# Optimization experiments

Hardware: AMD Instinct MI355X
Metric: run time of the kernel (lower is better)

Reference implementation:

```python
import jax, jax.numpy as jnp
import numpy as np

B, N, C, H, F = 4, 256, 256, 8, 64  # batch, nodes, in_channels, heads, n_hidden


def setup_inputs() -> dict:
    key = jax.random.key(0)
    k1, k2, k3, k4, k5 = jax.random.split(key, 5)
    x = jax.random.normal(k1, (B, N, C), jnp.float32)
    W_l = jax.random.normal(k2, (C, H * F), jnp.float32) / np.sqrt(C)
    W_r = jax.random.normal(k3, (C, H * F), jnp.float32) / np.sqrt(C)
    attn_w = jax.random.normal(k4, (F,), jnp.float32) / np.sqrt(F)
    adj = jax.random.randint(k5, (N, N, H), 0, 2, jnp.int32)
    # guarantee at least one unmasked head per (i, j) pair so the
    # softmax-over-heads (dim=-1 in the source) never sees all -inf
    adj = adj.at[:, :, 0].set(1)
    return {"x": x, "W_l": W_l, "W_r": W_r, "attn_w": attn_w, "adj": adj}


def reference(x, W_l, W_r, attn_w, adj):
    b, n, _ = x.shape
    g_l = (x @ W_l).reshape(b, n, H, F)
    g_r = (x @ W_r).reshape(b, n, H, F)
    # torch: g_l.repeat(1,n,1,1) + g_r.repeat_interleave(n,dim=1), then
    # view(b,n,n,h,f)  =>  g_sum[b,i,j,h,f] = g_r[b,i] + g_l[b,j]
    g_sum = g_r[:, :, None] + g_l[:, None, :]          # [b,i,j,h,f]
    e = jnp.einsum('bijhf,f->bijh', jax.nn.leaky_relu(g_sum, 0.2), attn_w)
    e = jnp.where(adj == 0, -jnp.inf, e)               # adj broadcasts over batch
    a = jax.nn.softmax(e, axis=-1)                     # softmax over heads, per source (dim=-1)
    out = jnp.einsum('bijh,bjhf->bihf', a, g_r)        # aggregate over neighbors j
    return out.reshape(b, n, H * F)                    # is_concat=True
```

## Files before the change

### kernel.cpp

```cpp
#include <hip/hip_runtime.h>
#include <hip/hip_bf16.h>

typedef _Float16 h2 __attribute__((ext_vector_type(2)));

constexpr int kB = 4, kN = 256, kC = 256, kH = 8, kF = 64, kHF = 512;
constexpr int kIPB = 4;
constexpr int kJS = 2;

union H2U { h2 h; unsigned int u; };

__global__ __launch_bounds__(256) void gat_gemm_kernel(
    const float* __restrict__ x,
    const float* __restrict__ Wl,
    const float* __restrict__ Wr,
    unsigned int* __restrict__ gl,
    unsigned int* __restrict__ gr,
    float* __restrict__ out)
{
    __shared__ float xs[4][kC];
    const int rowBase = blockIdx.x * 4;
    const float* Wm = (blockIdx.y == 0) ? Wl : Wr;
    unsigned int* gout = (blockIdx.y == 0) ? gl : gr;

    const int tid = threadIdx.x;

    if (blockIdx.y == 0) {
        float4 z = make_float4(0.f, 0.f, 0.f, 0.f);
        float4* o = (float4*)out + blockIdx.x * 512 + tid * 2;
        o[0] = z; o[1] = z;
    }

    {
        const int r = tid >> 6;
        const int kc = (tid & 63) * 4;
        *(float4*)&xs[r][kc] = *(const float4*)(x + (rowBase + r) * kC + kc);
    }
    __syncthreads();

    const int c0 = tid * 2;
    float acc[4][2];
#pragma unroll
    for (int r = 0; r < 4; ++r) { acc[r][0] = 0.f; acc[r][1] = 0.f; }

    float2 wv[4], wn[4];
#pragma unroll
    for (int kk = 0; kk < 4; ++kk)
        wv[kk] = *(const float2*)(Wm + kk * kHF + c0);

    for (int k = 0; k < kC; k += 4) {
        if (k + 4 < kC) {
#pragma unroll
            for (int kk = 0; kk < 4; ++kk)
                wn[kk] = *(const float2*)(Wm + (k + 4 + kk) * kHF + c0);
        }
#pragma unroll
        for (int r = 0; r < 4; ++r) {
            float4 xv = *(const float4*)&xs[r][k];
            acc[r][0] = fmaf(xv.x, wv[0].x, acc[r][0]);
            acc[r][1] = fmaf(xv.x, wv[0].y, acc[r][1]);
            acc[r][0] = fmaf(xv.y, wv[1].x, acc[r][0]);
            acc[r][1] = fmaf(xv.y, wv[1].y, acc[r][1]);
            acc[r][0] = fmaf(xv.z, wv[2].x, acc[r][0]);
            acc[r][1] = fmaf(xv.z, wv[2].y, acc[r][1]);
            acc[r][0] = fmaf(xv.w, wv[3].x, acc[r][0]);
            acc[r][1] = fmaf(xv.w, wv[3].y, acc[r][1]);
        }
#pragma unroll
        for (int kk = 0; kk < 4; ++kk) wv[kk] = wn[kk];
    }

#pragma unroll
    for (int r = 0; r < 4; ++r) {
        H2U p; p.h = (h2){(_Float16)acc[r][0], (_Float16)acc[r][1]};
        gout[((rowBase + r) * kHF + c0) >> 1] = p.u;
    }
}

__global__ __launch_bounds__(1024, 8) void gat_attn_kernel(
    const unsigned int* __restrict__ gl,
    const unsigned int* __restrict__ gr,
    const float* __restrict__ attn_w,
    const int* __restrict__ adj,
    float* __restrict__ out)
{
    __shared__ float red[8 * kIPB * kHF];
    __shared__ unsigned int msk[kN / kJS];

    const int bi0 = blockIdx.x * kIPB;
    const int i0 = bi0 & 255;
    const int j0 = blockIdx.y * (kN / kJS);
    const int tid = threadIdx.x;
    const int wv = tid >> 6;
    const int lane = tid & 63;
    const int h = lane >> 3;
    const int fg = lane & 7;

    if (tid < 512) {
        const int jj = tid & 127;
        const int ii = tid >> 7;
        const int* ap = adj + (i0 + ii) * (kN * kH) + (j0 + jj) * kH;
        uint4 a0 = *(const uint4*)ap;
        uint4 a1 = *(const uint4*)(ap + 4);
        unsigned int m = 0;
        m |= (a0.x != 0) << 0; m |= (a0.y != 0) << 1;
        m |= (a0.z != 0) << 2; m |= (a0.w != 0) << 3;
        m |= (a1.x != 0) << 4; m |= (a1.y != 0) << 5;
        m |= (a1.z != 0) << 6; m |= (a1.w != 0) << 7;
        ((unsigned char*)msk)[jj * 4 + ii] = (unsigned char)m;
    }

    h2 gri[kIPB][4];
#pragma unroll
    for (int ii = 0; ii < kIPB; ++ii) {
        uint4 pk = *(const uint4*)(gr + ((bi0 + ii) * 256 + h * 32 + fg * 4));
        H2U a0, a1, a2, a3;
        a0.u = pk.x; a1.u = pk.y; a2.u = pk.z; a3.u = pk.w;
        gri[ii][0] = a0.h; gri[ii][1] = a1.h; gri[ii][2] = a2.h; gri[ii][3] = a3.h;
    }
    h2 w2[4];
    {
        float4 wa = *(const float4*)(attn_w + fg * 8);
        float4 wb = *(const float4*)(attn_w + fg * 8 + 4);
        w2[0] = (h2){(_Float16)wa.x, (_Float16)wa.y};
        w2[1] = (h2){(_Float16)wa.z, (_Float16)wa.w};
        w2[2] = (h2){(_Float16)wb.x, (_Float16)wb.y};
        w2[3] = (h2){(_Float16)wb.z, (_Float16)wb.w};
    }

    h2 acc[kIPB][4];
#pragma unroll
    for (int ii = 0; ii < kIPB; ++ii)
#pragma unroll
        for (int q = 0; q < 4; ++q) acc[ii][q] = (h2){(_Float16)0.f, (_Float16)0.f};

    const h2 c02 = (h2){(_Float16)0.2f, (_Float16)0.2f};

    __syncthreads();

    unsigned int goff = (unsigned int)((bi0 >> 8) * (kN * 256)
                                       + (j0 + wv) * 256 + h * 32 + fg * 4);

    for (int it = 0; it < kN / kJS / 16; ++it) {
        const int jl = wv + it * 16;
        uint4 ga = *(const uint4*)(gl + goff);
        uint4 gb = *(const uint4*)(gr + goff);
        goff += 16 * 256;
        const unsigned int m = msk[jl];

        h2 gl2[4], gr2[4];
        { H2U t; t.u = ga.x; gl2[0] = t.h; t.u = ga.y; gl2[1] = t.h;
                 t.u = ga.z; gl2[2] = t.h; t.u = ga.w; gl2[3] = t.h;
                 t.u = gb.x; gr2[0] = t.h; t.u = gb.y; gr2[1] = t.h;
                 t.u = gb.z; gr2[2] = t.h; t.u = gb.w; gr2[3] = t.h; }

#pragma unroll
        for (int ii = 0; ii < kIPB; ++ii) {
            float e = 0.f;
#pragma unroll
            for (int q = 0; q < 4; ++q) {
                h2 s = gri[ii][q] + gl2[q];
                h2 u = __builtin_elementwise_max(s, c02 * s);
                e = __builtin_amdgcn_fdot2(u, w2[q], e, false);
            }
            e += __shfl_xor(e, 1);
            e += __shfl_xor(e, 2);
            e += __shfl_xor(e, 4);

            const unsigned int bit = (m >> (ii * 8 + h)) & 1u;
            e = bit ? e : -1e30f;

            float ex = __expf(e);
            float den = ex;
            den += __shfl_xor(den, 8);
            den += __shfl_xor(den, 16);
            den += __shfl_xor(den, 32);
            float a = ex * __builtin_amdgcn_rcpf(den);

            const h2 a2 = (h2){(_Float16)a, (_Float16)a};
#pragma unroll
            for (int q = 0; q < 4; ++q)
                acc[ii][q] = __builtin_elementwise_fma(a2, gr2[q], acc[ii][q]);
        }
    }

    if (wv >= 8) {
#pragma unroll
        for (int ii = 0; ii < kIPB; ++ii) {
            float* rp = &red[((wv - 8) * kIPB + ii) * kHF + lane * 8];
#pragma unroll
            for (int q = 0; q < 4; ++q) {
                float2 f = make_float2((float)acc[ii][q].x, (float)acc[ii][q].y);
                *(float2*)&rp[q * 2] = f;
            }
        }
    }
    __syncthreads();
    if (wv < 8) {
#pragma unroll
        for (int ii = 0; ii < kIPB; ++ii) {
            float* rp = &red[(wv * kIPB + ii) * kHF + lane * 8];
#pragma unroll
            for (int q = 0; q < 4; ++q) {
                float2 f = *(float2*)&rp[q * 2];
                f.x += (float)acc[ii][q].x;
                f.y += (float)acc[ii][q].y;
                *(float2*)&rp[q * 2] = f;
            }
        }
    }
    __syncthreads();

#pragma unroll
    for (int t = tid; t < kIPB * kHF; t += 1024) {
        const int ii = t >> 9;
        const int c  = t & 511;
        float s = 0.f;
#pragma unroll
        for (int w8 = 0; w8 < 8; ++w8)
            s += red[(w8 * kIPB + ii) * kHF + c];
        atomicAdd(&out[(bi0 + ii) * kHF + c], s);
    }
}

extern "C" void kernel_launch(void* const* d_in, const int* in_sizes, int n_in,
                              void* d_out, int out_size, void* d_ws, size_t ws_size,
                              hipStream_t stream) {
    const float* x  = (const float*)d_in[0];
    const float* Wl = (const float*)d_in[1];
    const float* Wr = (const float*)d_in[2];
    const float* aw = (const float*)d_in[3];
    const int* adj  = (const int*)d_in[4];

    unsigned int* gl = (unsigned int*)d_ws;
    unsigned int* gr = gl + (size_t)kB * kN * kHF / 2;

    dim3 g1(kB * kN / 4, 2);
    gat_gemm_kernel<<<g1, 256, 0, stream>>>(x, Wl, Wr, gl, gr, (float*)d_out);

    dim3 g2(kB * kN / kIPB, kJS);
    gat_attn_kernel<<<g2, 1024, 0, stream>>>(
        gl, gr, aw, adj, (float*)d_out);
}
```

Measured before the change: 112.7 us.

## Drop j-split and atomics in attention kernel; read x directly in GEMM

```diff
diff --git a/kernel.cpp b/kernel.cpp
--- a/kernel.cpp
+++ b/kernel.cpp
@@ -4,8 +4,7 @@
 typedef _Float16 h2 __attribute__((ext_vector_type(2)));
 
 constexpr int kB = 4, kN = 256, kC = 256, kH = 8, kF = 64, kHF = 512;
-constexpr int kIPB = 4;
-constexpr int kJS = 2;
+constexpr int kIPB = 2;
 
 union H2U { h2 h; unsigned int u; };
 
@@ -14,59 +13,41 @@
     const float* __restrict__ Wl,
     const float* __restrict__ Wr,
     unsigned int* __restrict__ gl,
-    unsigned int* __restrict__ gr,
-    float* __restrict__ out)
+    unsigned int* __restrict__ gr)
 {
-    __shared__ float xs[4][kC];
     const int rowBase = blockIdx.x * 4;
     const float* Wm = (blockIdx.y == 0) ? Wl : Wr;
     unsigned int* gout = (blockIdx.y == 0) ? gl : gr;
 
     const int tid = threadIdx.x;
-
-    if (blockIdx.y == 0) {
-        float4 z = make_float4(0.f, 0.f, 0.f, 0.f);
-        float4* o = (float4*)out + blockIdx.x * 512 + tid * 2;
-        o[0] = z; o[1] = z;
-    }
-
-    {
-        const int r = tid >> 6;
-        const int kc = (tid & 63) * 4;
-        *(float4*)&xs[r][kc] = *(const float4*)(x + (rowBase + r) * kC + kc);
-    }
-    __syncthreads();
-
     const int c0 = tid * 2;
+    const float* xr = x + rowBase * kC;
+
     float acc[4][2];
 #pragma unroll
     for (int r = 0; r < 4; ++r) { acc[r][0] = 0.f; acc[r][1] = 0.f; }
 
-    float2 wv[4], wn[4];
-#pragma unroll
-    for (int kk = 0; kk < 4; ++kk)
-        wv[kk] = *(const float2*)(Wm + kk * kHF + c0);
-
+#pragma unroll 2
     for (int k = 0; k < kC; k += 4) {
-        if (k + 4 < kC) {
-#pragma unroll
-            for (int kk = 0; kk < 4; ++kk)
-                wn[kk] = *(const float2*)(Wm + (k + 4 + kk) * kHF + c0);
-        }
+        float4 xv[4];
+#pragma unroll
+        for (int r = 0; r < 4; ++r)
+            xv[r] = *(const float4*)(xr + r * kC + k);
+        float2 wv[4];
+#pragma unroll
+        for (int kk = 0; kk < 4; ++kk)
+            wv[kk] = *(const float2*)(Wm + (k + kk) * kHF + c0);
 #pragma unroll
         for (int r = 0; r < 4; ++r) {
-            float4 xv = *(const float4*)&xs[r][k];
-            acc[r][0] = fmaf(xv.x, wv[0].x, acc[r][0]);
-            acc[r][1] = fmaf(xv.x, wv[0].y, acc[r][1]);
-            acc[r][0] = fmaf(xv.y, wv[1].x, acc[r][0]);
-            acc[r][1] = fmaf(xv.y, wv[1].y, acc[r][1]);
-            acc[r][0] = fmaf(xv.z, wv[2].x, acc[r][0]);
-            acc[r][1] = fmaf(xv.z, wv[2].y, acc[r][1]);
-            acc[r][0] = fmaf(xv.w, wv[3].x, acc[r][0]);
-            acc[r][1] = fmaf(xv.w, wv[3].y, acc[r][1]);
-        }
-#pragma unroll
-        for (int kk = 0; kk < 4; ++kk) wv[kk] = wn[kk];
+            acc[r][0] = fmaf(xv[r].x, wv[0].x, acc[r][0]);
+            acc[r][1] = fmaf(xv[r].x, wv[0].y, acc[r][1]);
+            acc[r][0] = fmaf(xv[r].y, wv[1].x, acc[r][0]);
+            acc[r][1] = fmaf(xv[r].y, wv[1].y, acc[r][1]);
+            acc[r][0] = fmaf(xv[r].z, wv[2].x, acc[r][0]);
+            acc[r][1] = fmaf(xv[r].z, wv[2].y, acc[r][1]);
+            acc[r][0] = fmaf(xv[r].w, wv[3].x, acc[r][0]);
+            acc[r][1] = fmaf(xv[r].w, wv[3].y, acc[r][1]);
+        }
     }
 
 #pragma unroll
@@ -76,29 +57,29 @@
     }
 }
 
-__global__ __launch_bounds__(1024, 8) void gat_attn_kernel(
+__global__ __launch_bounds__(512, 8) void gat_attn_kernel(
     const unsigned int* __restrict__ gl,
     const unsigned int* __restrict__ gr,
     const float* __restrict__ attn_w,
     const int* __restrict__ adj,
     float* __restrict__ out)
 {
-    __shared__ float red[8 * kIPB * kHF];
-    __shared__ unsigned int msk[kN / kJS];
+    __shared__ float red[4 * kIPB * kHF];
+    __shared__ unsigned short msk[kN];
 
     const int bi0 = blockIdx.x * kIPB;
+    const int b = bi0 >> 8;
     const int i0 = bi0 & 255;
-    const int j0 = blockIdx.y * (kN / kJS);
     const int tid = threadIdx.x;
     const int wv = tid >> 6;
     const int lane = tid & 63;
     const int h = lane >> 3;
     const int fg = lane & 7;
 
-    if (tid < 512) {
-        const int jj = tid & 127;
-        const int ii = tid >> 7;
-        const int* ap = adj + (i0 + ii) * (kN * kH) + (j0 + jj) * kH;
+    {
+        const int jj = tid & 255;
+        const int ii = tid >> 8;
+        const int* ap = adj + (i0 + ii) * (kN * kH) + jj * kH;
         uint4 a0 = *(const uint4*)ap;
         uint4 a1 = *(const uint4*)(ap + 4);
         unsigned int m = 0;
@@ -106,7 +87,7 @@
         m |= (a0.z != 0) << 2; m |= (a0.w != 0) << 3;
         m |= (a1.x != 0) << 4; m |= (a1.y != 0) << 5;
         m |= (a1.z != 0) << 6; m |= (a1.w != 0) << 7;
-        ((unsigned char*)msk)[jj * 4 + ii] = (unsigned char)m;
+        ((unsigned char*)msk)[jj * 2 + ii] = (unsigned char)m;
     }
 
     h2 gri[kIPB][4];
@@ -137,15 +118,16 @@
 
     __syncthreads();
 
-    unsigned int goff = (unsigned int)((bi0 >> 8) * (kN * 256)
-                                       + (j0 + wv) * 256 + h * 32 + fg * 4);
-
-    for (int it = 0; it < kN / kJS / 16; ++it) {
-        const int jl = wv + it * 16;
+    unsigned int goff = (unsigned int)(b * (kN * 256) + wv * 256
+                                       + h * 32 + fg * 4);
+
+#pragma unroll 2
+    for (int it = 0; it < kN / 8; ++it) {
+        const int j = wv + it * 8;
         uint4 ga = *(const uint4*)(gl + goff);
         uint4 gb = *(const uint4*)(gr + goff);
-        goff += 16 * 256;
-        const unsigned int m = msk[jl];
+        goff += 8 * 256;
+        const unsigned int m = msk[j];
 
         h2 gl2[4], gr2[4];
         { H2U t; t.u = ga.x; gl2[0] = t.h; t.u = ga.y; gl2[1] = t.h;
@@ -183,10 +165,10 @@
         }
     }
 
-    if (wv >= 8) {
+    if (wv >= 4) {
 #pragma unroll
         for (int ii = 0; ii < kIPB; ++ii) {
-            float* rp = &red[((wv - 8) * kIPB + ii) * kHF + lane * 8];
+            float* rp = &red[((wv - 4) * kIPB + ii) * kHF + lane * 8];
 #pragma unroll
             for (int q = 0; q < 4; ++q) {
                 float2 f = make_float2((float)acc[ii][q].x, (float)acc[ii][q].y);
@@ -195,7 +177,7 @@
         }
     }
     __syncthreads();
-    if (wv < 8) {
+    if (wv < 4) {
 #pragma unroll
         for (int ii = 0; ii < kIPB; ++ii) {
             float* rp = &red[(wv * kIPB + ii) * kHF + lane * 8];
@@ -211,14 +193,14 @@
     __syncthreads();
 
 #pragma unroll
-    for (int t = tid; t < kIPB * kHF; t += 1024) {
+    for (int t = tid; t < kIPB * kHF; t += 512) {
         const int ii = t >> 9;
         const int c  = t & 511;
         float s = 0.f;
 #pragma unroll
-        for (int w8 = 0; w8 < 8; ++w8)
-            s += red[(w8 * kIPB + ii) * kHF + c];
-        atomicAdd(&out[(bi0 + ii) * kHF + c], s);
+        for (int p = 0; p < 4; ++p)
+            s += red[(p * kIPB + ii) * kHF + c];
+        out[(bi0 + ii) * kHF + c] = s;
     }
 }
 
@@ -235,9 +217,8 @@
     unsigned int* gr = gl + (size_t)kB * kN * kHF / 2;
 
     dim3 g1(kB * kN / 4, 2);
-    gat_gemm_kernel<<<g1, 256, 0, stream>>>(x, Wl, Wr, gl, gr, (float*)d_out);
-
-    dim3 g2(kB * kN / kIPB, kJS);
-    gat_attn_kernel<<<g2, 1024, 0, stream>>>(
+    gat_gemm_kernel<<<g1, 256, 0, stream>>>(x, Wl, Wr, gl, gr);
+
+    gat_attn_kernel<<<kB * kN / kIPB, 512, 0, stream>>>(
         gl, gr, aw, adj, (float*)d_out);
 }
```

Result: no change. 111.6 us (-1.0%).

## Drop neighbor split in attention kernel, remove atomics, prefetch and fp16 reduce

Applied to the files above, without the earlier changes.

```diff
diff --git a/kernel.cpp b/kernel.cpp
--- a/kernel.cpp
+++ b/kernel.cpp
@@ -5,7 +5,6 @@
 
 constexpr int kB = 4, kN = 256, kC = 256, kH = 8, kF = 64, kHF = 512;
 constexpr int kIPB = 4;
-constexpr int kJS = 2;
 
 union H2U { h2 h; unsigned int u; };
 
@@ -14,8 +13,7 @@
     const float* __restrict__ Wl,
     const float* __restrict__ Wr,
     unsigned int* __restrict__ gl,
-    unsigned int* __restrict__ gr,
-    float* __restrict__ out)
+    unsigned int* __restrict__ gr)
 {
     __shared__ float xs[4][kC];
     const int rowBase = blockIdx.x * 4;
@@ -23,12 +21,6 @@
     unsigned int* gout = (blockIdx.y == 0) ? gl : gr;
 
     const int tid = threadIdx.x;
-
-    if (blockIdx.y == 0) {
-        float4 z = make_float4(0.f, 0.f, 0.f, 0.f);
-        float4* o = (float4*)out + blockIdx.x * 512 + tid * 2;
-        o[0] = z; o[1] = z;
-    }
 
     {
         const int r = tid >> 6;
@@ -76,29 +68,29 @@
     }
 }
 
-__global__ __launch_bounds__(1024, 8) void gat_attn_kernel(
+__global__ __launch_bounds__(1024, 4) void gat_attn_kernel(
     const unsigned int* __restrict__ gl,
     const unsigned int* __restrict__ gr,
     const float* __restrict__ attn_w,
     const int* __restrict__ adj,
     float* __restrict__ out)
 {
-    __shared__ float red[8 * kIPB * kHF];
-    __shared__ unsigned int msk[kN / kJS];
+    __shared__ unsigned int red[8 * kIPB * 256];
+    __shared__ unsigned int msk[kN];
 
     const int bi0 = blockIdx.x * kIPB;
+    const int b = bi0 >> 8;
     const int i0 = bi0 & 255;
-    const int j0 = blockIdx.y * (kN / kJS);
     const int tid = threadIdx.x;
     const int wv = tid >> 6;
     const int lane = tid & 63;
     const int h = lane >> 3;
     const int fg = lane & 7;
 
-    if (tid < 512) {
-        const int jj = tid & 127;
-        const int ii = tid >> 7;
-        const int* ap = adj + (i0 + ii) * (kN * kH) + (j0 + jj) * kH;
+    {
+        const int j = tid & 255;
+        const int ii = tid >> 8;
+        const int* ap = adj + (i0 + ii) * (kN * kH) + j * kH;
         uint4 a0 = *(const uint4*)ap;
         uint4 a1 = *(const uint4*)(ap + 4);
         unsigned int m = 0;
@@ -106,7 +98,7 @@
         m |= (a0.z != 0) << 2; m |= (a0.w != 0) << 3;
         m |= (a1.x != 0) << 4; m |= (a1.y != 0) << 5;
         m |= (a1.z != 0) << 6; m |= (a1.w != 0) << 7;
-        ((unsigned char*)msk)[jj * 4 + ii] = (unsigned char)m;
+        ((unsigned char*)msk)[j * 4 + ii] = (unsigned char)m;
     }
 
     h2 gri[kIPB][4];
@@ -137,15 +129,20 @@
 
     __syncthreads();
 
-    unsigned int goff = (unsigned int)((bi0 >> 8) * (kN * 256)
-                                       + (j0 + wv) * 256 + h * 32 + fg * 4);
-
-    for (int it = 0; it < kN / kJS / 16; ++it) {
-        const int jl = wv + it * 16;
-        uint4 ga = *(const uint4*)(gl + goff);
-        uint4 gb = *(const uint4*)(gr + goff);
-        goff += 16 * 256;
-        const unsigned int m = msk[jl];
+    unsigned int goff = (unsigned int)(b * (kN * 256) + wv * 256
+                                       + h * 32 + fg * 4);
+
+    uint4 ga = *(const uint4*)(gl + goff);
+    uint4 gb = *(const uint4*)(gr + goff);
+
+    for (int it = 0; it < 16; ++it) {
+        const int j = wv + it * 16;
+        const unsigned int offn = goff + 16 * 256;
+        uint4 ga_n = *(const uint4*)(gl + offn);
+        uint4 gb_n = *(const uint4*)(gr + offn);
+        goff = offn;
+
+        const unsigned int m = msk[j];
 
         h2 gl2[4], gr2[4];
         { H2U t; t.u = ga.x; gl2[0] = t.h; t.u = ga.y; gl2[1] = t.h;
@@ -181,44 +178,45 @@
             for (int q = 0; q < 4; ++q)
                 acc[ii][q] = __builtin_elementwise_fma(a2, gr2[q], acc[ii][q]);
         }
-    }
-
+
+        ga = ga_n; gb = gb_n;
+    }
+
+    const int ep = h * 32 + fg * 4;
     if (wv >= 8) {
 #pragma unroll
         for (int ii = 0; ii < kIPB; ++ii) {
-            float* rp = &red[((wv - 8) * kIPB + ii) * kHF + lane * 8];
+            unsigned int* rp = &red[((wv - 8) * kIPB + ii) * 256 + ep];
+#pragma unroll
+            for (int q = 0; q < 4; ++q) { H2U t; t.h = acc[ii][q]; rp[q] = t.u; }
+        }
+    }
+    __syncthreads();
+    if (wv < 8) {
+#pragma unroll
+        for (int ii = 0; ii < kIPB; ++ii) {
+            unsigned int* rp = &red[(wv * kIPB + ii) * 256 + ep];
 #pragma unroll
             for (int q = 0; q < 4; ++q) {
-                float2 f = make_float2((float)acc[ii][q].x, (float)acc[ii][q].y);
-                *(float2*)&rp[q * 2] = f;
+                H2U t; t.u = rp[q];
+                t.h = t.h + acc[ii][q];
+                rp[q] = t.u;
             }
         }
     }
     __syncthreads();
-    if (wv < 8) {
-#pragma unroll
-        for (int ii = 0; ii < kIPB; ++ii) {
-            float* rp = &red[(wv * kIPB + ii) * kHF + lane * 8];
-#pragma unroll
-            for (int q = 0; q < 4; ++q) {
-                float2 f = *(float2*)&rp[q * 2];
-                f.x += (float)acc[ii][q].x;
-                f.y += (float)acc[ii][q].y;
-                *(float2*)&rp[q * 2] = f;
-            }
-        }
-    }
-    __syncthreads();
-
-#pragma unroll
-    for (int t = tid; t < kIPB * kHF; t += 1024) {
-        const int ii = t >> 9;
-        const int c  = t & 511;
-        float s = 0.f;
-#pragma unroll
-        for (int w8 = 0; w8 < 8; ++w8)
-            s += red[(w8 * kIPB + ii) * kHF + c];
-        atomicAdd(&out[(bi0 + ii) * kHF + c], s);
+
+    {
+        const int ii = tid >> 8;
+        const int cp = tid & 255;
+        float2 s = make_float2(0.f, 0.f);
+#pragma unroll
+        for (int p = 0; p < 8; ++p) {
+            H2U t; t.u = red[(p * kIPB + ii) * 256 + cp];
+            s.x += (float)t.h.x;
+            s.y += (float)t.h.y;
+        }
+        *(float2*)&out[(bi0 + ii) * kHF + cp * 2] = s;
     }
 }
 
@@ -235,9 +233,8 @@
     unsigned int* gr = gl + (size_t)kB * kN * kHF / 2;
 
     dim3 g1(kB * kN / 4, 2);
-    gat_gemm_kernel<<<g1, 256, 0, stream>>>(x, Wl, Wr, gl, gr, (float*)d_out);
-
-    dim3 g2(kB * kN / kIPB, kJS);
-    gat_attn_kernel<<<g2, 1024, 0, stream>>>(
+    gat_gemm_kernel<<<g1, 256, 0, stream>>>(x, Wl, Wr, gl, gr);
+
+    gat_attn_kernel<<<kB * kN / kIPB, 1024, 0, stream>>>(
         gl, gr, aw, adj, (float*)d_out);
 }
```

After: 111.0 us. Within noise of the previous version (-1.5%).
